# Kernel optimization log

Hardware: AMD Instinct MI355X
Metric: run time of the kernel (lower is better)

The kernel has to match this reference:

```python
import jax, jax.numpy as jnp
import numpy as np

N, D, C, T, E = 8192, 512, 4, 8, 32768
H = D  # hidden_nf == input_nf == output_nf (required by the module's own shapes)


def _silu(x):
    return x * jax.nn.sigmoid(x)


def _lin(x, W, b):
    # torch Linear convention: W is [out, in]
    y = jnp.einsum('...i,oi->...o', x, W)
    return y + b


def setup_inputs() -> dict:
    key = jax.random.key(0)
    ks = jax.random.split(key, 20)
    s = 0.05  # keep activations in a sane range through stacked SiLU MLPs
    return {
        'h': jax.random.normal(ks[0], (N, D), jnp.float32),
        'coord': jax.random.normal(ks[1], (N, C, 3), jnp.float32),
        'edge_attr': jax.random.normal(ks[2], (T, E, 1), jnp.float32),
        'edge_index': jax.random.randint(ks[3], (T, 2, E), 0, N),
        'mW1': jax.random.normal(ks[4], (H, 2 * D + C * C + 1), jnp.float32) * s,
        'mb1': jnp.zeros((H,), jnp.float32),
        'mW2': jax.random.normal(ks[5], (H, H), jnp.float32) * s,
        'mb2': jnp.zeros((H,), jnp.float32),
        'nW1': jax.random.normal(ks[6], (H, H + D), jnp.float32) * s,
        'nb1': jnp.zeros((H,), jnp.float32),
        'nW2': jax.random.normal(ks[7], (D, H), jnp.float32) * s,
        'nb2': jnp.zeros((D,), jnp.float32),
        'eW1': jax.random.normal(ks[8], (H, H + 1 + H), jnp.float32) * s,
        'eb1': jnp.zeros((H,), jnp.float32),
        'eW2': jax.random.normal(ks[9], (1, H), jnp.float32) * s,
        'eb2': jnp.zeros((1,), jnp.float32),
        'relW': jax.random.normal(ks[10], (T, D, H), jnp.float32) * s,
        'cW1': jax.random.normal(ks[11], (T, H, H), jnp.float32) * s,
        'cb1': jnp.zeros((T, H), jnp.float32),
        'cW2': jax.random.normal(ks[12], (T, C, H), jnp.float32) * (s * 0.001),  # xavier gain=0.001
    }


def reference(h, coord, edge_attr, edge_index, mW1, mb1, mW2, mb2,
              nW1, nb1, nW2, nb2, eW1, eb1, eW2, eb2, relW, cW1, cb1, cW2):
    n, d = h.shape
    t, _, e = edge_index.shape
    c = coord.shape[1]
    row = edge_index[:, 0]  # [T,E]
    col = edge_index[:, 1]

    # coord2radial (per type, vectorized over type axis)
    cd = coord[row] - coord[col]                              # [T,E,C,3]
    radial = jnp.einsum('teca,teda->tecd', cd, cd)            # [T,E,C,C]
    # F.normalize(radial, dim=0): L2-normalize across the edge axis of each type
    nrm = jnp.sqrt(jnp.sum(radial * radial, axis=1, keepdims=True))
    radial = radial / jnp.maximum(nrm, 1e-12)

    # message_model (dropout = identity in eval)
    feat = jnp.concatenate([h[row], h[col], radial.reshape(t, e, c * c), edge_attr], axis=-1)
    msg = _silu(_lin(_silu(_lin(feat, mW1, mb1)), mW2, mb2))  # [T,E,H]

    # node_model: per-type segment_sum -> per-type relation linear -> sum
    seg = jax.vmap(lambda dta, ids: jax.ops.segment_sum(dta, ids, num_segments=n))(msg, row)  # [T,N,H]
    agg = jnp.einsum('tnh,tdh->nd', seg, relW)                # sum over types
    h_new = h + _lin(_silu(_lin(jnp.concatenate([h, agg], axis=-1), nW1, nb1)), nW2, nb2)

    # coord_model: per-type coord MLP weights, segment-mean over all types' edges
    hid = _silu(jnp.einsum('teh,tgh->teg', msg, cW1) + cb1[:, None, :])
    w = jnp.einsum('teg,tcg->tec', hid, cW2)                  # [T,E,C]
    trans = cd * w[..., None]                                 # [T,E,C,3]
    rows_flat = row.reshape(-1)
    sumv = jax.ops.segment_sum(trans.reshape(t * e, c, 3), rows_flat, num_segments=n)
    cnt = jax.ops.segment_sum(jnp.ones((t * e,), trans.dtype), rows_flat, num_segments=n)
    x_new = coord + sumv / jnp.maximum(cnt, 1.0)[:, None, None]

    # edge_model (note: forward passes edge_attr here, not the messages)
    ef = jnp.concatenate([h_new[row], edge_attr, h_new[col]], axis=-1)  # [T,E,H+1+H]
    m = _lin(_silu(_lin(ef, eW1, eb1)), eW2, eb2)             # [T,E,1]

    return (h_new, x_new, m)
```

## Files before the change

kernel.cpp:

```cpp
#include <hip/hip_runtime.h>
#include <cstdint>

#define NN 8192
#define DD 512
#define CC 4
#define TT 8
#define EE 32768
#define TE (TT*EE)

typedef __attribute__((ext_vector_type(8))) short short8v;
typedef __attribute__((ext_vector_type(4))) float f32x4;
typedef unsigned int uint;

constexpr int FLAG_SILU = 1, FLAG_RES = 2, FLAG_WEPI = 4, FLAG_BIAS_T = 8;

__device__ __forceinline__ float silu_f(float x) {
  return x * __builtin_amdgcn_rcpf(1.f + __expf(-x));
}

__device__ __forceinline__ unsigned short f2bf(float f) {
  uint u = __builtin_bit_cast(uint, f);
  u += 0x7fffu + ((u >> 16) & 1u);
  return (unsigned short)(u >> 16);
}
__device__ __forceinline__ float bf2f(unsigned short b) {
  uint u = ((uint)b) << 16;
  return __builtin_bit_cast(float, u);
}
__device__ __forceinline__ float bflo(uint u) { return __builtin_bit_cast(float, u << 16); }
__device__ __forceinline__ float bfhi(uint u) { return __builtin_bit_cast(float, u & 0xffff0000u); }
__device__ __forceinline__ uint packbf(float a, float b) {
  return (uint)f2bf(a) | ((uint)f2bf(b) << 16);
}

__device__ __forceinline__ float wave_sum(float v) {
#pragma unroll
  for (int off = 32; off; off >>= 1) v += __shfl_xor(v, off);
  return v;
}

__device__ __forceinline__ void gload16(const void* g, void* l) {
  __builtin_amdgcn_global_load_lds(
      (const __attribute__((address_space(1))) void*)g,
      (__attribute__((address_space(3))) void*)l, 16, 0, 0);
}

__device__ __forceinline__ int xcd_swz(int i, int nwg) {
  return (i & 7) * (nwg >> 3) + (i >> 3);
}

struct AgDirect { const unsigned short* p; int K;
  __device__ const void* ptr(int m, int k, int) const { return p + (size_t)m * K + k; } };

struct AgHcat { const unsigned short* hb; const unsigned short* ab;
  __device__ const void* ptr(int m, int k, int) const {
    return (k < 512) ? (const void*)(hb + ((size_t)m << 9) + k)
                     : (const void*)(ab + ((size_t)m << 9) + (k - 512)); } };

struct AgSegG { const unsigned short* seg;
  __device__ const void* ptr(int m, int k, int) const {
    return seg + (((size_t)(k >> 9) * NN + m) << 9) + (k & 511); } };

struct BgDirect { const unsigned short* p; int K;
  __device__ const void* ptr(int o, int k, int) const { return p + (size_t)o * K + k; } };

struct BgRelG { const unsigned short* w;
  __device__ const void* ptr(int o, int k, int) const {
    return w + (((size_t)(k >> 9) * 512 + o) << 9) + (k & 511); } };

struct BgPerT { const unsigned short* w;
  __device__ const void* ptr(int o, int k, int tt) const {
    return w + (((size_t)tt << 18) + ((size_t)o << 9)) + k; } };

template<class AG, class BG>
__global__ __launch_bounds__(256)
void mgemm_k(AG ag, BG bg, int K, int tbase, int lognx,
             const float* __restrict__ bias, const float* __restrict__ res,
             float* __restrict__ outF, unsigned short* __restrict__ outB, int ldo, int flags)
{
  __shared__ __align__(16) unsigned short SM[128 * 136];
  unsigned short* As = SM;
  unsigned short* Bs = SM + 128 * 64;
  const int swz = xcd_swz(blockIdx.x, gridDim.x);
  const int xb = swz & ((1 << lognx) - 1), yb = swz >> lognx;
  const int m0 = yb * 128, o0 = xb * 128;
  const int tt = tbase + (m0 >> 15);
  const int tid = threadIdx.x, wave = tid >> 6, lane = tid & 63;
  const int wr = (wave >> 1) * 64, wc = (wave & 1) * 64;
  const int rs = lane >> 3, sl = lane & 7;

  f32x4 acc[4][4];
#pragma unroll
  for (int i = 0; i < 4; ++i)
#pragma unroll
    for (int j = 0; j < 4; ++j) acc[i][j] = (f32x4)0.f;

  for (int k0 = 0; k0 < K; k0 += 64) {
#pragma unroll
    for (int i = 0; i < 4; ++i) {
      int r = i * 32 + wave * 8 + rs;
      int slot = sl ^ (r & 7);
      gload16(ag.ptr(m0 + r, k0 + slot * 8, tt), &As[(i * 32 + wave * 8) * 64]);
    }
#pragma unroll
    for (int i = 0; i < 4; ++i) {
      int r = i * 32 + wave * 8 + rs;
      int slot = sl ^ (r & 7);
      gload16(bg.ptr(o0 + r, k0 + slot * 8, tt), &Bs[(i * 32 + wave * 8) * 64]);
    }
    __syncthreads();
    short8v a[4][2], b[4][2];
#pragma unroll
    for (int mi = 0; mi < 4; ++mi)
#pragma unroll
      for (int s = 0; s < 2; ++s) {
        int row = wr + mi * 16 + (lane & 15);
        int slot = (s * 4 + (lane >> 4)) ^ (row & 7);
        a[mi][s] = *(const short8v*)&As[row * 64 + slot * 8];
      }
#pragma unroll
    for (int ni = 0; ni < 4; ++ni)
#pragma unroll
      for (int s = 0; s < 2; ++s) {
        int row = wc + ni * 16 + (lane & 15);
        int slot = (s * 4 + (lane >> 4)) ^ (row & 7);
        b[ni][s] = *(const short8v*)&Bs[row * 64 + slot * 8];
      }
#pragma unroll
    for (int s = 0; s < 2; ++s)
#pragma unroll
      for (int mi = 0; mi < 4; ++mi)
#pragma unroll
        for (int ni = 0; ni < 4; ++ni)
          acc[mi][ni] = __builtin_amdgcn_mfma_f32_16x16x32_bf16(a[mi][s], b[ni][s], acc[mi][ni], 0, 0, 0);
    __syncthreads();
  }

  const int r4 = (lane >> 4) * 4, cl = lane & 15;
  if (outB && !outF) {
    unsigned short* Ep = SM;
#pragma unroll
    for (int mi = 0; mi < 4; ++mi)
#pragma unroll
      for (int ni = 0; ni < 4; ++ni)
#pragma unroll
        for (int rg = 0; rg < 4; ++rg) {
          int row = wr + mi * 16 + r4 + rg;
          int col = wc + ni * 16 + cl;
          float v = acc[mi][ni][rg];
          if (bias) v += (flags & FLAG_BIAS_T) ? bias[tt * 512 + o0 + col] : bias[o0 + col];
          if (flags & FLAG_SILU) v = silu_f(v);
          Ep[row * 136 + col] = f2bf(v);
        }
    __syncthreads();
#pragma unroll
    for (int p = 0; p < 8; ++p) {
      int idx = p * 256 + tid;
      int row = idx >> 4, ch = idx & 15;
      short8v vv = *(const short8v*)&Ep[row * 136 + ch * 8];
      *(short8v*)(outB + (size_t)(m0 + row) * ldo + o0 + ch * 8) = vv;
    }
    return;
  }
#pragma unroll
  for (int mi = 0; mi < 4; ++mi)
#pragma unroll
    for (int ni = 0; ni < 4; ++ni)
#pragma unroll
      for (int rg = 0; rg < 4; ++rg) {
        int row = m0 + wr + mi * 16 + r4 + rg;
        int col = o0 + wc + ni * 16 + cl;
        float v = acc[mi][ni][rg];
        if (bias) v += (flags & FLAG_BIAS_T) ? bias[tt * 512 + col] : bias[col];
        if (flags & FLAG_SILU) v = silu_f(v);
        if (flags & FLAG_RES) v += res[(size_t)row * ldo + col];
        if (outF) outF[(size_t)row * ldo + col] = v;
        if (outB) outB[(size_t)row * ldo + col] = f2bf(v);
      }
}

template<class AG, class BG>
__global__ __launch_bounds__(512)
void mgemm2_k(AG ag, BG bg, int K, int tbase,
              const float* __restrict__ bias,
              unsigned short* __restrict__ outB, int flags,
              const float* __restrict__ cw2, float* __restrict__ wpart, int wstride)
{
  __shared__ __align__(16) unsigned short SM[128 * 136];
  unsigned short* As = SM;
  unsigned short* Bs = SM + 128 * 64;
  const int swz = xcd_swz(blockIdx.x, gridDim.x);
  const int xb = swz & 3, yb = swz >> 2;
  const int m0 = yb * 128, o0 = xb * 128;
  const int tt = tbase + (m0 >> 15);
  const int tid = threadIdx.x, wave = tid >> 6, lane = tid & 63;
  const int wr = (wave >> 1) * 32, wc = (wave & 1) * 64;
  const int rs = lane >> 3, sl = lane & 7;

  f32x4 acc[2][4];
#pragma unroll
  for (int i = 0; i < 2; ++i)
#pragma unroll
    for (int j = 0; j < 4; ++j) acc[i][j] = (f32x4)0.f;

  for (int k0 = 0; k0 < K; k0 += 64) {
#pragma unroll
    for (int i = 0; i < 2; ++i) {
      int r = i * 64 + wave * 8 + rs;
      int slot = sl ^ (r & 7);
      gload16(ag.ptr(m0 + r, k0 + slot * 8, tt), &As[(i * 64 + wave * 8) * 64]);
    }
#pragma unroll
    for (int i = 0; i < 2; ++i) {
      int r = i * 64 + wave * 8 + rs;
      int slot = sl ^ (r & 7);
      gload16(bg.ptr(o0 + r, k0 + slot * 8, tt), &Bs[(i * 64 + wave * 8) * 64]);
    }
    __syncthreads();
    short8v a[2][2], b[4][2];
#pragma unroll
    for (int mi = 0; mi < 2; ++mi)
#pragma unroll
      for (int s = 0; s < 2; ++s) {
        int row = wr + mi * 16 + (lane & 15);
        int slot = (s * 4 + (lane >> 4)) ^ (row & 7);
        a[mi][s] = *(const short8v*)&As[row * 64 + slot * 8];
      }
#pragma unroll
    for (int ni = 0; ni < 4; ++ni)
#pragma unroll
      for (int s = 0; s < 2; ++s) {
        int row = wc + ni * 16 + (lane & 15);
        int slot = (s * 4 + (lane >> 4)) ^ (row & 7);
        b[ni][s] = *(const short8v*)&Bs[row * 64 + slot * 8];
      }
#pragma unroll
    for (int s = 0; s < 2; ++s)
#pragma unroll
      for (int mi = 0; mi < 2; ++mi)
#pragma unroll
        for (int ni = 0; ni < 4; ++ni)
          acc[mi][ni] = __builtin_amdgcn_mfma_f32_16x16x32_bf16(a[mi][s], b[ni][s], acc[mi][ni], 0, 0, 0);
    __syncthreads();
  }

  const int r4 = (lane >> 4) * 4, cl = lane & 15;
  if (flags & FLAG_WEPI) {
    const int slice = xb * 2 + (wave & 1);
    const float* cw2t = cw2 + tt * 2048;
    const float* bt = bias + tt * 512;
#pragma unroll
    for (int mi = 0; mi < 2; ++mi) {
      float sc[4][4];
#pragma unroll
      for (int rg = 0; rg < 4; ++rg)
#pragma unroll
        for (int c = 0; c < 4; ++c) sc[rg][c] = 0.f;
#pragma unroll
      for (int ni = 0; ni < 4; ++ni) {
        int col = o0 + wc + ni * 16 + cl;
        float c0 = cw2t[col], c1 = cw2t[512 + col], c2 = cw2t[1024 + col], c3 = cw2t[1536 + col];
        float bb = bt[col];
#pragma unroll
        for (int rg = 0; rg < 4; ++rg) {
          float v = silu_f(acc[mi][ni][rg] + bb);
          sc[rg][0] += v * c0; sc[rg][1] += v * c1; sc[rg][2] += v * c2; sc[rg][3] += v * c3;
        }
      }
#pragma unroll
      for (int rg = 0; rg < 4; ++rg)
#pragma unroll
        for (int c = 0; c < 4; ++c) {
          float s = sc[rg][c];
          s += __shfl_xor(s, 1); s += __shfl_xor(s, 2);
          s += __shfl_xor(s, 4); s += __shfl_xor(s, 8);
          sc[rg][c] = s;
        }
      if (cl == 0) {
        int p = m0 + wr + mi * 16 + r4;
#pragma unroll
        for (int rg = 0; rg < 4; ++rg) {
          float4 o = make_float4(sc[rg][0], sc[rg][1], sc[rg][2], sc[rg][3]);
          *(float4*)&wpart[(((size_t)slice * wstride) + p + rg) * 4] = o;
        }
      }
    }
    return;
  }
  unsigned short* Ep = SM;
#pragma unroll
  for (int mi = 0; mi < 2; ++mi)
#pragma unroll
    for (int ni = 0; ni < 4; ++ni)
#pragma unroll
      for (int rg = 0; rg < 4; ++rg) {
        int row = wr + mi * 16 + r4 + rg;
        int col = wc + ni * 16 + cl;
        float v = acc[mi][ni][rg];
        v += bias[o0 + col];
        if (flags & FLAG_SILU) v = silu_f(v);
        Ep[row * 136 + col] = f2bf(v);
      }
  __syncthreads();
#pragma unroll
  for (int p = 0; p < 4; ++p) {
    int idx = p * 512 + tid;
    int row = idx >> 4, ch = idx & 15;
    short8v vv = *(const short8v*)&Ep[row * 136 + ch * 8];
    *(short8v*)(outB + (size_t)(m0 + row) * 512 + o0 + ch * 8) = vv;
  }
}

__global__ __launch_bounds__(256)
void prep_k(const float* h, const float* mW2, const float* nW1, const float* nW2,
            const float* relW, const float* cW1, const float* mW1, const float* eW1,
            const float* mb1, const float* eb1,
            unsigned short* hb, unsigned short* mW2b, unsigned short* nW1b,
            unsigned short* nW2b, unsigned short* relWb, unsigned short* cW1b,
            unsigned short* mW1pq, unsigned short* eGc, unsigned short* mW1t,
            float* wea, float* pqb, float* ggb)
{
  int i = blockIdx.x * 256 + threadIdx.x;
  if (i < 4194304) { hb[i] = f2bf(h[i]); return; }
  i -= 4194304;
  if (i < 262144) { mW2b[i] = f2bf(mW2[i]); return; }
  i -= 262144;
  if (i < 524288) { nW1b[i] = f2bf(nW1[i]); return; }
  i -= 524288;
  if (i < 262144) { nW2b[i] = f2bf(nW2[i]); return; }
  i -= 262144;
  if (i < 2097152) { relWb[i] = f2bf(relW[i]); return; }
  i -= 2097152;
  if (i < 2097152) { cW1b[i] = f2bf(cW1[i]); return; }
  i -= 2097152;
  if (i < 262144) { int r = i >> 9, k = i & 511; mW1pq[i] = f2bf(mW1[(size_t)r * 1041 + k]); return; }
  i -= 262144;
  if (i < 262144) { int r = i >> 9, k = i & 511; mW1pq[262144 + i] = f2bf(mW1[(size_t)r * 1041 + 512 + k]); return; }
  i -= 262144;
  if (i < 262144) { int r = i >> 9, k = i & 511; eGc[i] = f2bf(eW1[(size_t)r * 1025 + k]); return; }
  i -= 262144;
  if (i < 262144) { int r = i >> 9, k = i & 511; eGc[262144 + i] = f2bf(eW1[(size_t)r * 1025 + 513 + k]); return; }
  i -= 262144;
  if (i < 8704) { int j = i >> 9, c = i & 511; mW1t[i] = f2bf(mW1[(size_t)c * 1041 + 1024 + j]); return; }
  i -= 8704;
  if (i < 512) { wea[i] = eW1[(size_t)i * 1025 + 512]; return; }
  i -= 512;
  if (i < 1024) {
    pqb[i] = (i < 512) ? mb1[i] : 0.f;
    ggb[i] = (i < 512) ? eb1[i] : 0.f;
  }
}

__global__ __launch_bounds__(256)
void hist_k(const int* __restrict__ eidx, int* __restrict__ deg) {
  int id = blockIdx.x * 256 + threadIdx.x;
  int t = id >> 15, e = id & (EE - 1);
  atomicAdd(&deg[(t << 13) + eidx[(t << 16) + e]], 1);
}

__global__ __launch_bounds__(256)
void scan_k(const int* __restrict__ deg, int* __restrict__ off, int* __restrict__ cursor) {
  int t = blockIdx.x, tid = threadIdx.x;
  __shared__ int lds[256];
  int base = 0;
  for (int ch = 0; ch < 32; ++ch) {
    int i = ch * 256 + tid;
    int v = deg[(t << 13) + i];
    __syncthreads();
    lds[tid] = v;
    __syncthreads();
    for (int s = 1; s < 256; s <<= 1) {
      int x = (tid >= s) ? lds[tid - s] : 0;
      __syncthreads();
      if (tid >= s) lds[tid] += x;
      __syncthreads();
    }
    int excl = base + lds[tid] - v;
    off[(t << 13) + i] = excl;
    cursor[(t << 13) + i] = excl;
    base += lds[255];
  }
}

__global__ __launch_bounds__(256)
void scatcd_k(const int* __restrict__ eidx, const float* __restrict__ ea,
              const float* __restrict__ coord, int* __restrict__ cursor,
              int* __restrict__ order, int* __restrict__ rowS, int* __restrict__ colS,
              float* __restrict__ eaS, float* __restrict__ cd,
              float* __restrict__ radial, float* __restrict__ pnrm)
{
  int m = blockIdx.x * 256 + threadIdx.x;
  int t = m >> 15, e = m & (EE - 1);
  int r = eidx[(t << 16) + e], c = eidx[(t << 16) + EE + e];
  int pos = atomicAdd(&cursor[(t << 13) + r], 1);
  size_t s = ((size_t)t << 15) + pos;
  order[s] = e; rowS[s] = r; colS[s] = c; eaS[s] = ea[m];
  const float4* cv4 = (const float4*)coord;
  float4 A0 = cv4[r * 3], A1 = cv4[r * 3 + 1], A2 = cv4[r * 3 + 2];
  float4 B0 = cv4[c * 3], B1 = cv4[c * 3 + 1], B2 = cv4[c * 3 + 2];
  float d[12] = {A0.x-B0.x, A0.y-B0.y, A0.z-B0.z, A0.w-B0.w,
                 A1.x-B1.x, A1.y-B1.y, A1.z-B1.z, A1.w-B1.w,
                 A2.x-B2.x, A2.y-B2.y, A2.z-B2.z, A2.w-B2.w};
  float4* cdv = (float4*)cd;
  cdv[s*3+0] = make_float4(d[0],d[1],d[2],d[3]);
  cdv[s*3+1] = make_float4(d[4],d[5],d[6],d[7]);
  cdv[s*3+2] = make_float4(d[8],d[9],d[10],d[11]);
  float rad[16], sq[16];
#pragma unroll
  for (int ci = 0; ci < 4; ++ci)
#pragma unroll
    for (int di = 0; di < 4; ++di) {
      float v = d[ci*3]*d[di*3] + d[ci*3+1]*d[di*3+1] + d[ci*3+2]*d[di*3+2];
      rad[ci*4+di] = v; sq[ci*4+di] = v * v;
    }
  float4* rv = (float4*)radial;
#pragma unroll
  for (int i = 0; i < 4; ++i)
    rv[s*4+i] = make_float4(rad[i*4], rad[i*4+1], rad[i*4+2], rad[i*4+3]);
#pragma unroll
  for (int i = 0; i < 16; ++i) sq[i] = wave_sum(sq[i]);
  __shared__ float red[4][16];
  int wv = threadIdx.x >> 6, lane = threadIdx.x & 63;
  if (lane == 0) {
#pragma unroll
    for (int i = 0; i < 16; ++i) red[wv][i] = sq[i];
  }
  __syncthreads();
  if (threadIdx.x < 16)
    pnrm[blockIdx.x * 16 + threadIdx.x] =
        red[0][threadIdx.x] + red[1][threadIdx.x] + red[2][threadIdx.x] + red[3][threadIdx.x];
}

__global__ __launch_bounds__(128)
void nrmred_k(const float* __restrict__ pnrm, float* __restrict__ nrm) {
  int t = threadIdx.x >> 4, j = threadIdx.x & 15;
  float s = 0.f;
  for (int b = 0; b < 128; ++b) s += pnrm[((t * 128 + b) << 4) + j];
  nrm[(t << 4) + j] = s;
}

__global__ __launch_bounds__(256)
void tails_k(const float* __restrict__ radial, const float* __restrict__ nrm,
             const float* __restrict__ eaS, unsigned short* __restrict__ tailm)
{
  int m = blockIdx.x * 256 + threadIdx.x;
  int t = m >> 15;
  unsigned short tmp[24];
#pragma unroll
  for (int j = 0; j < 16; ++j) {
    float r = radial[(size_t)m * 16 + j] / fmaxf(sqrtf(nrm[(t << 4) + j]), 1e-12f);
    tmp[j] = f2bf(r);
  }
  tmp[16] = f2bf(eaS[m]);
#pragma unroll
  for (int j = 17; j < 24; ++j) tmp[j] = 0;
  uint4* dst = (uint4*)(tailm + (size_t)m * 24);
  dst[0] = ((const uint4*)tmp)[0];
  dst[1] = ((const uint4*)tmp)[1];
  dst[2] = ((const uint4*)tmp)[2];
}

__global__ __launch_bounds__(256)
void msg1f_k(const unsigned short* __restrict__ PQ, const unsigned short* __restrict__ Wt,
             const unsigned short* __restrict__ tailm_g,
             const int* __restrict__ rowS_g, const int* __restrict__ colS_g,
             unsigned short* __restrict__ out)
{
  int tid = threadIdx.x;
  int e0 = xcd_swz(blockIdx.x, gridDim.x) * 8;
  uint wreg[17];
#pragma unroll
  for (int j = 0; j < 17; ++j) wreg[j] = *(const uint*)(Wt + j * 512 + tid * 2);
  for (int i = 0; i < 8; ++i) {
    int p = e0 + i;
    int r = rowS_g[p], c = colS_g[p];
    uint pv = *(const uint*)(PQ + ((size_t)r << 10) + tid * 2);
    uint qv = *(const uint*)(PQ + ((size_t)c << 10) + 512 + tid * 2);
    uint4 t0 = *(const uint4*)(tailm_g + (size_t)p * 24);
    uint4 t1 = *(const uint4*)(tailm_g + (size_t)p * 24 + 8);
    uint  t2 = *(const uint*)(tailm_g + (size_t)p * 24 + 16);
    float tl[17] = {bflo(t0.x), bfhi(t0.x), bflo(t0.y), bfhi(t0.y),
                    bflo(t0.z), bfhi(t0.z), bflo(t0.w), bfhi(t0.w),
                    bflo(t1.x), bfhi(t1.x), bflo(t1.y), bfhi(t1.y),
                    bflo(t1.z), bfhi(t1.z), bflo(t1.w), bfhi(t1.w),
                    bflo(t2)};
    float s0 = bflo(pv) + bflo(qv);
    float s1 = bfhi(pv) + bfhi(qv);
#pragma unroll
    for (int j = 0; j < 17; ++j) {
      s0 += tl[j] * bflo(wreg[j]); s1 += tl[j] * bfhi(wreg[j]);
    }
    *(uint*)(out + ((size_t)p << 9) + tid * 2) = packbf(silu_f(s0), silu_f(s1));
  }
}

__global__ __launch_bounds__(256)
void gsum_k(const unsigned short* __restrict__ msg, const int* __restrict__ offb,
            const int* __restrict__ deg, int tbase, unsigned short* __restrict__ segt)
{
  int l = xcd_swz(blockIdx.x, gridDim.x);
  int tloc = l >> 13, n = l & (NN - 1), tid = threadIdx.x;
  int t = tbase + tloc;
  int start = offb[(t << 13) + n], d = deg[(t << 13) + n];
  float s0 = 0.f, s1 = 0.f;
  const unsigned short* base = msg + (((size_t)tloc << 15) << 9);
  for (int j = 0; j < d; ++j) {
    uint v = *(const uint*)(base + ((size_t)(start + j) << 9) + tid * 2);
    s0 += bflo(v); s1 += bfhi(v);
  }
  *(uint*)(segt + (((size_t)tloc * NN + n) << 9) + tid * 2) = packbf(s0, s1);
}

__global__ __launch_bounds__(256)
void wsum_k(const float* __restrict__ wpart, float* __restrict__ wsum_out, int wstride) {
  int id = xcd_swz(blockIdx.x, gridDim.x) * 256 + threadIdx.x;
  float4 a = (float4){0.f, 0.f, 0.f, 0.f};
#pragma unroll
  for (int s = 0; s < 8; ++s) {
    float4 v = *(const float4*)&wpart[(((size_t)s * wstride) + id) * 4];
    a.x += v.x; a.y += v.y; a.z += v.z; a.w += v.w;
  }
  *(float4*)&wsum_out[(size_t)id * 4] = a;
}

__global__ __launch_bounds__(256)
void trxn_k(const float* __restrict__ coord, const float* __restrict__ cd,
            const float* __restrict__ wsum, const int* __restrict__ offb,
            const int* __restrict__ deg, float* __restrict__ xout)
{
  int id = blockIdx.x * 256 + threadIdx.x;
  int n = id / 12, j = id - n * 12, ci = j / 3;
  float s = 0.f; int cnt = 0;
#pragma unroll
  for (int t = 0; t < 8; ++t) {
    int o = offb[(t << 13) + n], d = deg[(t << 13) + n];
    size_t p = ((size_t)t << 15) + o;
    for (int k = 0; k < d; ++k)
      s += cd[(p + k) * 12 + j] * wsum[(p + k) * 4 + ci];
    cnt += d;
  }
  xout[id] = coord[id] + s / fmaxf((float)cnt, 1.f);
}

__global__ __launch_bounds__(256)
void mout_k(const unsigned short* __restrict__ GG,
            const float* __restrict__ eW2, const float* __restrict__ wea,
            const float* __restrict__ eb2, const float* __restrict__ eaS,
            const int* __restrict__ rowS, const int* __restrict__ colS,
            const int* __restrict__ order, float* __restrict__ out_m)
{
  int wid = xcd_swz(blockIdx.x, gridDim.x) * 4 + (threadIdx.x >> 6);
  int lane = threadIdx.x & 63;
  int t = wid >> 15;
  int r = rowS[wid], c = colS[wid];
  float eav = eaS[wid];
  short8v gv  = *(const short8v*)(GG + ((size_t)r << 10) + lane * 8);
  short8v gcv = *(const short8v*)(GG + ((size_t)c << 10) + 512 + lane * 8);
  const float4* w4 = (const float4*)(eW2 + lane * 8);
  const float4* a4 = (const float4*)(wea + lane * 8);
  float4 w0 = w4[0], w1 = w4[1], a0 = a4[0], a1 = a4[1];
  float wv8[8] = {w0.x,w0.y,w0.z,w0.w,w1.x,w1.y,w1.z,w1.w};
  float av8[8] = {a0.x,a0.y,a0.z,a0.w,a1.x,a1.y,a1.z,a1.w};
  float s = 0.f;
#pragma unroll
  for (int j = 0; j < 8; ++j)
    s += wv8[j] * silu_f(bf2f((unsigned short)gv[j]) + bf2f((unsigned short)gcv[j]) + eav * av8[j]);
  s = wave_sum(s);
  if (lane == 0) out_m[((size_t)t << 15) + order[wid]] = s + eb2[0];
}

extern "C" void kernel_launch(void* const* d_in, const int* in_sizes, int n_in,
                              void* d_out, int out_size, void* d_ws, size_t ws_size,
                              hipStream_t stream)
{
  const float* h     = (const float*)d_in[0];
  const float* coord = (const float*)d_in[1];
  const float* ea    = (const float*)d_in[2];
  const int*   eidx  = (const int*)  d_in[3];
  const float* mW1   = (const float*)d_in[4];
  const float* mb1   = (const float*)d_in[5];
  const float* mW2   = (const float*)d_in[6];
  const float* mb2   = (const float*)d_in[7];
  const float* nW1   = (const float*)d_in[8];
  const float* nb1   = (const float*)d_in[9];
  const float* nW2   = (const float*)d_in[10];
  const float* nb2   = (const float*)d_in[11];
  const float* eW1   = (const float*)d_in[12];
  const float* eb1   = (const float*)d_in[13];
  const float* eW2   = (const float*)d_in[14];
  const float* eb2   = (const float*)d_in[15];
  const float* relW  = (const float*)d_in[16];
  const float* cW1   = (const float*)d_in[17];
  const float* cb1   = (const float*)d_in[18];
  const float* cW2   = (const float*)d_in[19];

  float* out   = (float*)d_out;
  float* out_h = out;
  float* out_x = out + (size_t)NN * DD;
  float* out_m = out_x + (size_t)NN * CC * 3;

  char* ws = (char*)d_ws;
  size_t off = 0;
  auto alloc = [&](size_t bytes) -> void* {
    void* p = ws + off; off += (bytes + 255) & ~(size_t)255; return p;
  };
  float* cd     = (float*)alloc((size_t)TE * 12 * 4);
  unsigned short* tailm = (unsigned short*)alloc((size_t)TE * 24 * 2);
  float* agg    = (float*)alloc((size_t)NN * 512 * 4);
  unsigned short* h_bf  = (unsigned short*)alloc((size_t)NN * 512 * 2);
  unsigned short* hn_bf = (unsigned short*)alloc((size_t)NN * 512 * 2);
  unsigned short* PQb   = (unsigned short*)alloc((size_t)NN * 1024 * 2);
  unsigned short* GGb   = PQb;
  unsigned short* mW1pq = (unsigned short*)alloc((size_t)1024 * 512 * 2);
  unsigned short* mW1t  = (unsigned short*)alloc((size_t)17 * 512 * 2);
  unsigned short* mW2b  = (unsigned short*)alloc((size_t)512 * 512 * 2);
  unsigned short* nW1b  = (unsigned short*)alloc((size_t)512 * 1024 * 2);
  unsigned short* nW2b  = (unsigned short*)alloc((size_t)512 * 512 * 2);
  unsigned short* eGc   = (unsigned short*)alloc((size_t)1024 * 512 * 2);
  float* weab   = (float*)alloc(512 * 4);
  float* pqbias = (float*)alloc(1024 * 4);
  float* ggbias = (float*)alloc(1024 * 4);
  unsigned short* relWb = (unsigned short*)alloc((size_t)TT * 512 * 512 * 2);
  unsigned short* cW1b  = (unsigned short*)alloc((size_t)TT * 512 * 512 * 2);
  int* deg     = (int*)alloc((size_t)TT * NN * 4);
  int* offb    = (int*)alloc((size_t)TT * NN * 4);
  int* cursor  = (int*)alloc((size_t)TT * NN * 4);
  int* order   = (int*)alloc((size_t)TE * 4);
  int* rowS    = (int*)alloc((size_t)TE * 4);
  int* colS    = (int*)alloc((size_t)TE * 4);
  float* eaS   = (float*)alloc((size_t)TE * 4);
  float* wsumb = (float*)alloc((size_t)TE * 4 * 4);
  float* pnrm  = (float*)alloc((size_t)(TE / 256) * 16 * 4);
  float* nrm   = (float*)alloc((size_t)TT * 16 * 4);

  const size_t perG = (size_t)EE * 512 * 2 * 2 + (size_t)NN * 512 * 2 + (size_t)8 * EE * 16;
  int G = 4;
  while (G > 1 && off + (size_t)G * perG + (1 << 20) > ws_size) G >>= 1;
  unsigned short* bufA = (unsigned short*)alloc((size_t)G * EE * 512 * 2);
  unsigned short* bufB = (unsigned short*)alloc((size_t)G * EE * 512 * 2);
  unsigned short* segt = (unsigned short*)alloc((size_t)G * NN * 512 * 2);
  float* wpart = (float*)alloc((size_t)8 * G * EE * 4 * 4);
  unsigned short* aggb = segt;
  float* radial = (float*)bufA;

  hipMemsetAsync(deg, 0, (size_t)TT * NN * 4, stream);
  hipMemsetAsync(agg, 0, (size_t)NN * 512 * 4, stream);

  prep_k<<<41000, 256, 0, stream>>>(h, mW2, nW1, nW2, relW, cW1, mW1, eW1, mb1, eb1,
      h_bf, mW2b, nW1b, nW2b, relWb, cW1b, mW1pq, eGc, mW1t, weab, pqbias, ggbias);

  hist_k<<<TE / 256, 256, 0, stream>>>(eidx, deg);
  scan_k<<<TT, 256, 0, stream>>>(deg, offb, cursor);
  scatcd_k<<<TE / 256, 256, 0, stream>>>(eidx, ea, coord, cursor,
      order, rowS, colS, eaS, cd, radial, pnrm);
  nrmred_k<<<1, 128, 0, stream>>>(pnrm, nrm);
  tails_k<<<TE / 256, 256, 0, stream>>>(radial, nrm, eaS, tailm);

  mgemm_k<<<512, 256, 0, stream>>>(AgDirect{h_bf, 512}, BgDirect{mW1pq, 512}, 512, 0, 3,
      pqbias, nullptr, nullptr, PQb, 1024, 0);

  for (int g = 0; g < TT / G; ++g) {
    const int tbase = g * G;
    const size_t gb = (size_t)tbase << 15;
    msg1f_k<<<(G * EE) / 8, 256, 0, stream>>>(PQb, mW1t, tailm + gb * 24,
        rowS + gb, colS + gb, bufA);
    mgemm2_k<<<4 * (G * EE / 128), 512, 0, stream>>>(AgDirect{bufA, 512},
        BgDirect{mW2b, 512}, 512, tbase,
        mb2, bufB, FLAG_SILU, nullptr, nullptr, 0);
    gsum_k<<<G * NN, 256, 0, stream>>>(bufB, offb, deg, tbase, segt);
    bool last = (g == TT / G - 1);
    mgemm_k<<<4 * (NN / 128), 256, 0, stream>>>(AgSegG{segt},
        BgRelG{relWb + ((size_t)tbase << 18)}, G * 512, 0, 2,
        nullptr, agg, agg, last ? aggb : nullptr, 512, FLAG_RES);
    mgemm2_k<<<4 * (G * EE / 128), 512, 0, stream>>>(AgDirect{bufB, 512},
        BgPerT{cW1b}, 512, tbase,
        cb1, nullptr, FLAG_SILU | FLAG_WEPI | FLAG_BIAS_T, cW2, wpart, G * EE);
    wsum_k<<<(G * EE) / 256, 256, 0, stream>>>(wpart, wsumb + gb * 4, G * EE);
  }

  trxn_k<<<(NN * 12) / 256, 256, 0, stream>>>(coord, cd, wsumb, offb, deg, out_x);

  mgemm_k<<<4 * (NN / 128), 256, 0, stream>>>(AgHcat{h_bf, aggb}, BgDirect{nW1b, 1024}, 1024, 0, 2,
      nb1, nullptr, nullptr, bufA, 512, FLAG_SILU);
  mgemm_k<<<4 * (NN / 128), 256, 0, stream>>>(AgDirect{bufA, 512}, BgDirect{nW2b, 512}, 512, 0, 2,
      nb2, h, out_h, hn_bf, 512, FLAG_RES);

  mgemm_k<<<512, 256, 0, stream>>>(AgDirect{hn_bf, 512}, BgDirect{eGc, 512}, 512, 0, 3,
      ggbias, nullptr, nullptr, GGb, 1024, 0);
  mout_k<<<TE / 4, 256, 0, stream>>>(GGb, eW2, weab, eb2, eaS, rowS, colS, order, out_m);

  (void)in_sizes; (void)n_in; (void)out_size; (void)ws_size;
}
```

Baseline: 1.233 ms.

## Fuse coord weight reduction via atomics, rescan degrees per-thread, batch mout edges

The cW1 GEMM epilogue now accumulates per-row coordinate weights into wsumb with float atomicAdd instead of writing 8 partial slices. This removes the separate wsum_k reduction pass and the wpart buffer, at the cost of a memset and atomic contention across 8 column slices. The degree scan now has each thread own 32 contiguous entries and runs a single block-wide scan, replacing 32 serial chunk scans. mout_k handles two edges per wave to get more memory-level parallelism. Atomic accumulation makes the summation order nondeterministic.

```diff
diff --git a/kernel.cpp b/kernel.cpp
--- a/kernel.cpp
+++ b/kernel.cpp
@@ -184,7 +184,7 @@
 void mgemm2_k(AG ag, BG bg, int K, int tbase,
               const float* __restrict__ bias,
               unsigned short* __restrict__ outB, int flags,
-              const float* __restrict__ cw2, float* __restrict__ wpart, int wstride)
+              const float* __restrict__ cw2, float* __restrict__ wsum_out)
 {
   __shared__ __align__(16) unsigned short SM[128 * 136];
   unsigned short* As = SM;
@@ -246,7 +246,6 @@
 
   const int r4 = (lane >> 4) * 4, cl = lane & 15;
   if (flags & FLAG_WEPI) {
-    const int slice = xb * 2 + (wave & 1);
     const float* cw2t = cw2 + tt * 2048;
     const float* bt = bias + tt * 512;
 #pragma unroll
@@ -276,14 +275,8 @@
           s += __shfl_xor(s, 4); s += __shfl_xor(s, 8);
           sc[rg][c] = s;
         }
-      if (cl == 0) {
-        int p = m0 + wr + mi * 16 + r4;
-#pragma unroll
-        for (int rg = 0; rg < 4; ++rg) {
-          float4 o = make_float4(sc[rg][0], sc[rg][1], sc[rg][2], sc[rg][3]);
-          *(float4*)&wpart[(((size_t)slice * wstride) + p + rg) * 4] = o;
-        }
-      }
+      size_t gp = ((size_t)tbase << 15) + m0 + wr + mi * 16 + r4 + (cl >> 2);
+      atomicAdd(&wsum_out[gp * 4 + (cl & 3)], sc[cl >> 2][cl & 3]);
     }
     return;
   }
@@ -361,24 +354,23 @@
 __global__ __launch_bounds__(256)
 void scan_k(const int* __restrict__ deg, int* __restrict__ off, int* __restrict__ cursor) {
   int t = blockIdx.x, tid = threadIdx.x;
+  int base = (t << 13) + tid * 32;
+  int loc[32]; int s = 0;
+#pragma unroll
+  for (int i = 0; i < 32; ++i) { loc[i] = deg[base + i]; s += loc[i]; }
   __shared__ int lds[256];
-  int base = 0;
-  for (int ch = 0; ch < 32; ++ch) {
-    int i = ch * 256 + tid;
-    int v = deg[(t << 13) + i];
+  lds[tid] = s;
+  __syncthreads();
+  for (int st = 1; st < 256; st <<= 1) {
+    int x = (tid >= st) ? lds[tid - st] : 0;
     __syncthreads();
-    lds[tid] = v;
+    lds[tid] += x;
     __syncthreads();
-    for (int s = 1; s < 256; s <<= 1) {
-      int x = (tid >= s) ? lds[tid - s] : 0;
-      __syncthreads();
-      if (tid >= s) lds[tid] += x;
-      __syncthreads();
-    }
-    int excl = base + lds[tid] - v;
-    off[(t << 13) + i] = excl;
-    cursor[(t << 13) + i] = excl;
-    base += lds[255];
+  }
+  int run = lds[tid] - s;
+#pragma unroll
+  for (int i = 0; i < 32; ++i) {
+    off[base + i] = run; cursor[base + i] = run; run += loc[i];
   }
 }
 
@@ -512,18 +504,6 @@
 }
 
 __global__ __launch_bounds__(256)
-void wsum_k(const float* __restrict__ wpart, float* __restrict__ wsum_out, int wstride) {
-  int id = xcd_swz(blockIdx.x, gridDim.x) * 256 + threadIdx.x;
-  float4 a = (float4){0.f, 0.f, 0.f, 0.f};
-#pragma unroll
-  for (int s = 0; s < 8; ++s) {
-    float4 v = *(const float4*)&wpart[(((size_t)s * wstride) + id) * 4];
-    a.x += v.x; a.y += v.y; a.z += v.z; a.w += v.w;
-  }
-  *(float4*)&wsum_out[(size_t)id * 4] = a;
-}
-
-__global__ __launch_bounds__(256)
 void trxn_k(const float* __restrict__ coord, const float* __restrict__ cd,
             const float* __restrict__ wsum, const int* __restrict__ offb,
             const int* __restrict__ deg, float* __restrict__ xout)
@@ -549,24 +529,34 @@
             const int* __restrict__ rowS, const int* __restrict__ colS,
             const int* __restrict__ order, float* __restrict__ out_m)
 {
-  int wid = xcd_swz(blockIdx.x, gridDim.x) * 4 + (threadIdx.x >> 6);
+  int wbase = xcd_swz(blockIdx.x, gridDim.x) * 8 + (threadIdx.x >> 6) * 2;
   int lane = threadIdx.x & 63;
-  int t = wid >> 15;
-  int r = rowS[wid], c = colS[wid];
-  float eav = eaS[wid];
-  short8v gv  = *(const short8v*)(GG + ((size_t)r << 10) + lane * 8);
-  short8v gcv = *(const short8v*)(GG + ((size_t)c << 10) + 512 + lane * 8);
+  int w0i = wbase, w1i = wbase + 1;
+  int r0 = rowS[w0i], c0 = colS[w0i], r1 = rowS[w1i], c1 = colS[w1i];
+  float ea0 = eaS[w0i], ea1 = eaS[w1i];
+  short8v gv0  = *(const short8v*)(GG + ((size_t)r0 << 10) + lane * 8);
+  short8v gcv0 = *(const short8v*)(GG + ((size_t)c0 << 10) + 512 + lane * 8);
+  short8v gv1  = *(const short8v*)(GG + ((size_t)r1 << 10) + lane * 8);
+  short8v gcv1 = *(const short8v*)(GG + ((size_t)c1 << 10) + 512 + lane * 8);
   const float4* w4 = (const float4*)(eW2 + lane * 8);
   const float4* a4 = (const float4*)(wea + lane * 8);
   float4 w0 = w4[0], w1 = w4[1], a0 = a4[0], a1 = a4[1];
   float wv8[8] = {w0.x,w0.y,w0.z,w0.w,w1.x,w1.y,w1.z,w1.w};
   float av8[8] = {a0.x,a0.y,a0.z,a0.w,a1.x,a1.y,a1.z,a1.w};
-  float s = 0.f;
-#pragma unroll
-  for (int j = 0; j < 8; ++j)
-    s += wv8[j] * silu_f(bf2f((unsigned short)gv[j]) + bf2f((unsigned short)gcv[j]) + eav * av8[j]);
-  s = wave_sum(s);
-  if (lane == 0) out_m[((size_t)t << 15) + order[wid]] = s + eb2[0];
+  float s0 = 0.f, s1 = 0.f;
+#pragma unroll
+  for (int j = 0; j < 8; ++j) {
+    s0 += wv8[j] * silu_f(bf2f((unsigned short)gv0[j]) + bf2f((unsigned short)gcv0[j]) + ea0 * av8[j]);
+    s1 += wv8[j] * silu_f(bf2f((unsigned short)gv1[j]) + bf2f((unsigned short)gcv1[j]) + ea1 * av8[j]);
+  }
+  s0 = wave_sum(s0);
+  s1 = wave_sum(s1);
+  if (lane == 0) {
+    float eb = eb2[0];
+    int t0 = w0i >> 15, t1 = w1i >> 15;
+    out_m[((size_t)t0 << 15) + order[w0i]] = s0 + eb;
+    out_m[((size_t)t1 << 15) + order[w1i]] = s1 + eb;
+  }
 }
 
 extern "C" void kernel_launch(void* const* d_in, const int* in_sizes, int n_in,
@@ -633,18 +623,18 @@
   float* pnrm  = (float*)alloc((size_t)(TE / 256) * 16 * 4);
   float* nrm   = (float*)alloc((size_t)TT * 16 * 4);
 
-  const size_t perG = (size_t)EE * 512 * 2 * 2 + (size_t)NN * 512 * 2 + (size_t)8 * EE * 16;
+  const size_t perG = (size_t)EE * 512 * 2 * 2 + (size_t)NN * 512 * 2;
   int G = 4;
   while (G > 1 && off + (size_t)G * perG + (1 << 20) > ws_size) G >>= 1;
   unsigned short* bufA = (unsigned short*)alloc((size_t)G * EE * 512 * 2);
   unsigned short* bufB = (unsigned short*)alloc((size_t)G * EE * 512 * 2);
   unsigned short* segt = (unsigned short*)alloc((size_t)G * NN * 512 * 2);
-  float* wpart = (float*)alloc((size_t)8 * G * EE * 4 * 4);
   unsigned short* aggb = segt;
   float* radial = (float*)bufA;
 
   hipMemsetAsync(deg, 0, (size_t)TT * NN * 4, stream);
   hipMemsetAsync(agg, 0, (size_t)NN * 512 * 4, stream);
+  hipMemsetAsync(wsumb, 0, (size_t)TE * 4 * 4, stream);
 
   prep_k<<<41000, 256, 0, stream>>>(h, mW2, nW1, nW2, relW, cW1, mW1, eW1, mb1, eb1,
       h_bf, mW2b, nW1b, nW2b, relWb, cW1b, mW1pq, eGc, mW1t, weab, pqbias, ggbias);
@@ -666,7 +656,7 @@
         rowS + gb, colS + gb, bufA);
     mgemm2_k<<<4 * (G * EE / 128), 512, 0, stream>>>(AgDirect{bufA, 512},
         BgDirect{mW2b, 512}, 512, tbase,
-        mb2, bufB, FLAG_SILU, nullptr, nullptr, 0);
+        mb2, bufB, FLAG_SILU, nullptr, nullptr);
     gsum_k<<<G * NN, 256, 0, stream>>>(bufB, offb, deg, tbase, segt);
     bool last = (g == TT / G - 1);
     mgemm_k<<<4 * (NN / 128), 256, 0, stream>>>(AgSegG{segt},
@@ -674,8 +664,7 @@
         nullptr, agg, agg, last ? aggb : nullptr, 512, FLAG_RES);
     mgemm2_k<<<4 * (G * EE / 128), 512, 0, stream>>>(AgDirect{bufB, 512},
         BgPerT{cW1b}, 512, tbase,
-        cb1, nullptr, FLAG_SILU | FLAG_WEPI | FLAG_BIAS_T, cW2, wpart, G * EE);
-    wsum_k<<<(G * EE) / 256, 256, 0, stream>>>(wpart, wsumb + gb * 4, G * EE);
+        cb1, nullptr, FLAG_SILU | FLAG_WEPI | FLAG_BIAS_T, cW2, wsumb);
   }
 
   trxn_k<<<(NN * 12) / 256, 256, 0, stream>>>(coord, cd, wsumb, offb, deg, out_x);
@@ -687,7 +676,7 @@
 
   mgemm_k<<<512, 256, 0, stream>>>(AgDirect{hn_bf, 512}, BgDirect{eGc, 512}, 512, 0, 3,
       ggbias, nullptr, nullptr, GGb, 1024, 0);
-  mout_k<<<TE / 4, 256, 0, stream>>>(GGb, eW2, weab, eb2, eaS, rowS, colS, order, out_m);
+  mout_k<<<TE / 8, 256, 0, stream>>>(GGb, eW2, weab, eb2, eaS, rowS, colS, order, out_m);
 
   (void)in_sizes; (void)n_in; (void)out_size; (void)ws_size;
 }
```

After: 1.189 ms. 3.6% less time.
